# Kernel optimization log

Hardware: AMD Instinct MI355X
Metric: run time of the kernel (lower is better)

Reference implementation:

```python
import jax, jax.numpy as jnp
import numpy as np

L = 512       # sequence length
N_AA = 21     # amino-acid alphabet size
D = 128       # per-residue substitution embedding dim
N1 = 256
N2 = 256


def setup_inputs() -> dict:
    key = jax.random.key(0)
    k1, k2, k3 = jax.random.split(key, 3)
    X1 = jax.random.randint(k1, (N1, L), 0, N_AA)
    X2 = jax.random.randint(k2, (N2, L), 0, N_AA)
    W = jax.random.normal(k3, (L * N_AA, N_AA * D), dtype=jnp.float32) * 0.02
    b = jnp.zeros((N_AA * D,), jnp.float32)
    w_param = jnp.zeros((L * (L - 1) // 2,), jnp.float32)
    a = jnp.ones((1,), jnp.float32)
    return {"X1": X1, "X2": X2, "W": W, "b": b, "w_param": w_param, "a": a}


def _network(X, W, b):
    # one-hot + linear stand-in for self.network; outputs (n, n_aa, d)
    n = X.shape[0]
    oh = jax.nn.one_hot(X, N_AA, dtype=W.dtype).reshape(n, -1)  # (n, L*n_aa)
    return (oh @ W + b).reshape(n, N_AA, -1)


def _wdk(subs, w):
    # torch: (subs[:, graph] * w).sum(2) * subs, summed over dim 1
    # graph[i] = arange(L), so this equals subs @ w^T contracted with subs:
    # out[..] = sum_i sum_j subs[.., i] * w[i, j] * subs[.., j]
    return jnp.einsum('...i,ij,...j->...', subs, w, subs)


def reference(X1, X2, W, b, w_param, a):
    n1, Lx = X1.shape
    n2 = X2.shape[0]

    # symmetric pairwise weight matrix; diagonal stays 0 -> sigmoid(0)=0.5
    i_x, i_y = np.tril_indices(Lx, k=-1)
    wm = jnp.zeros((Lx, Lx), W.dtype).at[i_x, i_y].set(w_param).at[i_y, i_x].set(w_param)
    w = jax.nn.sigmoid(wm)

    # per-sequence substitution matrices S = E E^T, (n, n_aa, n_aa)
    E1 = _network(X1, W, b)
    S1 = jnp.einsum('nad,nbd->nab', E1, E1)
    E2 = _network(X2, W, b)
    S2 = jnp.einsum('nad,nbd->nab', E2, E2)

    r1 = jnp.arange(n1)
    r2 = jnp.arange(n2)

    # self terms: subs[n, l] = S[n, X[n,l], X[n,l]]
    d1 = S1[r1[:, None], X1, X1]                  # (n1, L)
    k1 = _wdk(d1, w)[:, None]                     # (n1, 1)
    d2 = S2[r2[:, None], X2, X2]                  # (n2, L)
    k2 = _wdk(d2, w)[None, :]                     # (1, n2)

    # cross terms: average of the two sequences' S, gathered directly
    # (avoids materializing the (n1*n2, n_aa, n_aa) averaged S tensor)
    g1 = S1[r1[:, None, None], X1[:, None, :], X2[None, :, :]]  # (n1, n2, L)
    g2 = S2[r2[None, :, None], X1[:, None, :], X2[None, :, :]]  # (n1, n2, L)
    subs = 0.5 * (g1 + g2)

    K = _wdk(subs, w)                             # (n1, n2)
    K = K / jnp.sqrt(k1) / jnp.sqrt(k2)
    return (a ** 2) * K
```

## Files before the change

kernel.cpp:

```cpp
#include <hip/hip_runtime.h>
#include <cstdint>
#include <cstddef>

typedef __attribute__((ext_vector_type(8))) __bf16 bf16x8;
typedef __attribute__((ext_vector_type(4))) float f32x4;
typedef __attribute__((ext_vector_type(16))) float f32x16;

__device__ __forceinline__ unsigned short f2b(float x) {
    uint32_t u = __float_as_uint(x);
    u += 0x7FFFu + ((u >> 16) & 1u);
    return (unsigned short)(u >> 16);
}
__device__ __forceinline__ float b2f(unsigned short h) {
    return __uint_as_float(((uint32_t)h) << 16);
}

#define L_SEQ 512
#define N_AA 21
#define DDIM 128
#define NCOL 2688
#define NSEQ 512
#define TBSTRIDE 448
#define KTOT 10752
#define ZCH 12
#define KBTOT 672
#define KBCH 56

#define PB_WBZ   14112
#define PB_EINIT 5376
#define PB_REPACK 1024
#define PB_WBUILD 1024
#define PB_ABZ   2688
#define PB_TOTAL (PB_WBZ + PB_EINIT + PB_REPACK + PB_WBUILD + PB_ABZ)

__global__ __launch_bounds__(256) void prep_kernel(const int* X1, const int* X2,
                                                   const float* W, const float* bvec, const float* wp,
                                                   uint8_t* X8,
                                                   float* w32, unsigned short* wswz,
                                                   float* E, unsigned short* Wbz, unsigned short* Abz) {
    int bid = blockIdx.x;
    int t = threadIdx.x;
    if (bid < PB_WBZ) {
        int f = bid * 4 + (t >> 6);
        int lane = t & 63, lr = lane & 31, hf = lane >> 5;
        int cb = f / KBTOT, kb = f - cb * KBTOT;
        const float* src = W + (size_t)(kb * 16 + hf * 8) * NCOL + cb * 32 + lr;
        union { uint4 q; unsigned short s[8]; } o;
#pragma unroll
        for (int j = 0; j < 8; ++j) o.s[j] = f2b(src[(size_t)j * NCOL]);
        *(uint4*)&Wbz[(size_t)f * 512 + lane * 8] = o.q;
        return;
    }
    bid -= PB_WBZ;
    if (bid < PB_EINIT) {
        int e = bid * 256 + t;
        E[e] = bvec[e % NCOL];
        return;
    }
    bid -= PB_EINIT;
    if (bid < PB_REPACK) {
        int e = bid * 256 + t;
        if (e < 131072) X8[e] = (uint8_t)X1[e];
        else            X8[e] = (uint8_t)X2[e - 131072];
        return;
    }
    bid -= PB_REPACK;
    if (bid < PB_WBUILD) {
        int e = bid * 256 + t;
        int p = e >> 9, q = e & 511;
        float x = 0.0f;
        if (p > q)      x = wp[p * (p - 1) / 2 + q];
        else if (p < q) x = wp[q * (q - 1) / 2 + p];
        float s = 1.0f / (1.0f + expf(-x));
        w32[e] = s;
        int nb = p >> 5, lr = p & 31;
        int kb = q >> 4, hf = (q >> 3) & 1, j = q & 7;
        wswz[(size_t)((nb * 32 + kb) * 512) + (hf * 32 + lr) * 8 + j] = f2b(s);
        return;
    }
    bid -= PB_WBUILD;
    {
        int f = bid * 4 + (t >> 6);
        int lane = t & 63, lr = lane & 31, hf = lane >> 5;
        int mb = f / KBTOT, kb = f - mb * KBTOT;
        int m = mb * 32 + lr;
        const int* Xrow = (m < 256) ? (X1 + (size_t)m * L_SEQ) : (X2 + (size_t)(m - 256) * L_SEQ);
        int k0 = kb * 16 + hf * 8;
        union { uint4 q; unsigned short s[8]; } o;
#pragma unroll
        for (int j = 0; j < 8; ++j) {
            int k = k0 + j;
            int l = k / N_AA;
            int aa = k - l * N_AA;
            o.s[j] = (Xrow[l] == aa) ? (unsigned short)0x3F80u : (unsigned short)0u;
        }
        *(uint4*)&Abz[(size_t)f * 512 + lane * 8] = o.q;
    }
}

__global__ __launch_bounds__(256, 4) void e_mfma_v2(const unsigned short* Abz, const unsigned short* Wbz, float* E) {
    int lin = blockIdx.x;
    int s = ((lin & 7) * 126) + (lin >> 3);
    int cx = s % 21;
    int rem = s / 21;
    int my = rem & 3;
    int kz = rem >> 2;

    int t = threadIdx.x, wid = t >> 6, lane = t & 63;
    int lr = lane & 31, hf = lane >> 5;

    int kb0 = kz * KBCH;
    int mb0 = my * 4 + (wid & 1) * 2;
    int cb0 = cx * 4 + (wid >> 1) * 2;

    const unsigned short* Ap0 = Abz + ((size_t)(mb0 * KBTOT + kb0)) * 512 + lane * 8;
    const unsigned short* Ap1 = Ap0 + (size_t)KBTOT * 512;
    const unsigned short* Bp0 = Wbz + ((size_t)(cb0 * KBTOT + kb0)) * 512 + lane * 8;
    const unsigned short* Bp1 = Bp0 + (size_t)KBTOT * 512;

    f32x16 acc00, acc01, acc10, acc11;
#pragma unroll
    for (int r = 0; r < 16; ++r) { acc00[r] = 0.f; acc01[r] = 0.f; acc10[r] = 0.f; acc11[r] = 0.f; }

#pragma unroll 2
    for (int kb = 0; kb < KBCH; ++kb) {
        bf16x8 a0 = *(const bf16x8*)(Ap0 + kb * 512);
        bf16x8 a1 = *(const bf16x8*)(Ap1 + kb * 512);
        bf16x8 b0 = *(const bf16x8*)(Bp0 + kb * 512);
        bf16x8 b1 = *(const bf16x8*)(Bp1 + kb * 512);
        acc00 = __builtin_amdgcn_mfma_f32_32x32x16_bf16(a0, b0, acc00, 0, 0, 0);
        acc01 = __builtin_amdgcn_mfma_f32_32x32x16_bf16(a0, b1, acc01, 0, 0, 0);
        acc10 = __builtin_amdgcn_mfma_f32_32x32x16_bf16(a1, b0, acc10, 0, 0, 0);
        acc11 = __builtin_amdgcn_mfma_f32_32x32x16_bf16(a1, b1, acc11, 0, 0, 0);
    }

#pragma unroll
    for (int r = 0; r < 16; ++r) {
        int row = (r & 3) + 8 * (r >> 2) + 4 * hf;
        float* base = E + (size_t)(mb0 * 32 + row) * NCOL + cb0 * 32 + lr;
        atomicAdd(base, acc00[r]);
        atomicAdd(base + 32, acc01[r]);
        atomicAdd(base + (size_t)32 * NCOL, acc10[r]);
        atomicAdd(base + (size_t)32 * NCOL + 32, acc11[r]);
    }
}

__global__ __launch_bounds__(256) void t_kernel(const float* E, unsigned short* Tb, float* Tdiag) {
    __shared__ float4 Es4[21 * 33];
    int t = threadIdx.x, n = blockIdx.x;
    for (int e = t; e < 21 * 32; e += 256) {
        int r = e >> 5, d = e & 31;
        Es4[r * 33 + d] = *(const float4*)(E + (size_t)n * NCOL + r * 128 + d * 4);
    }
    __syncthreads();
    for (int e = t; e < 441; e += 256) {
        int r = e / 21, c = e - r * 21;
        const float4* ar = &Es4[r * 33];
        const float4* br = &Es4[c * 33];
        float s = 0.f;
#pragma unroll 8
        for (int d = 0; d < 32; ++d) {
            float4 a = ar[d], b = br[d];
            s += a.x * b.x + a.y * b.y + a.z * b.z + a.w * b.w;
        }
        Tb[(size_t)n * TBSTRIDE + e] = f2b(0.5f * s);
        if (r == c) Tdiag[n * 24 + r] = s;
    }
}

__global__ __launch_bounds__(256) void k_kernel(const uint8_t* X8, const float* Tdiag, const float* w32, float* kinv) {
    __shared__ __align__(16) float dvec[4][512];
    __shared__ float Td[4][21];
    __shared__ float red[4][256];
    int t = threadIdx.x, n0 = blockIdx.x * 4;
    if (t < 84) Td[t / 21][t % 21] = Tdiag[(size_t)(n0 + t / 21) * 24 + (t % 21)];
    __syncthreads();
    for (int e = t; e < 2048; e += 256) {
        int nn = e >> 9, l = e & 511;
        dvec[nn][l] = Td[nn][X8[(size_t)(n0 + nn) * 512 + l]];
    }
    __syncthreads();
    float p0 = 0.f, p1 = 0.f, p2 = 0.f, p3 = 0.f;
    for (int p = t; p < 512; p += 256) {
        const float4* wr4 = (const float4*)(w32 + (size_t)p * 512);
        float d0 = 0.f, d1 = 0.f, d2 = 0.f, d3 = 0.f;
        for (int q = 0; q < 128; ++q) {
            float4 wv = wr4[q];
            float4 a = ((const float4*)dvec[0])[q];
            float4 b = ((const float4*)dvec[1])[q];
            float4 c = ((const float4*)dvec[2])[q];
            float4 d = ((const float4*)dvec[3])[q];
            d0 += wv.x * a.x + wv.y * a.y + wv.z * a.z + wv.w * a.w;
            d1 += wv.x * b.x + wv.y * b.y + wv.z * b.z + wv.w * b.w;
            d2 += wv.x * c.x + wv.y * c.y + wv.z * c.z + wv.w * c.w;
            d3 += wv.x * d.x + wv.y * d.y + wv.z * d.z + wv.w * d.w;
        }
        p0 += dvec[0][p] * d0;
        p1 += dvec[1][p] * d1;
        p2 += dvec[2][p] * d2;
        p3 += dvec[3][p] * d3;
    }
    red[0][t] = p0; red[1][t] = p1; red[2][t] = p2; red[3][t] = p3;
    __syncthreads();
    for (int s = 128; s > 0; s >>= 1) {
        if (t < s) {
            red[0][t] += red[0][t + s];
            red[1][t] += red[1][t + s];
            red[2][t] += red[2][t + s];
            red[3][t] += red[3][t + s];
        }
        __syncthreads();
    }
    if (t < 4) kinv[n0 + t] = 1.0f / sqrtf(red[t][0]);
}

__global__ __launch_bounds__(512, 6) void k4_kernel(const uint8_t* X8, const unsigned short* Tb,
                                                    const unsigned short* wswz, const float* kinv,
                                                    const float* Ainp, float* out) {
    __shared__ unsigned short Sh[32 * 520];
    __shared__ unsigned short Ts1h[4 * TBSTRIDE];
    __shared__ unsigned short Ts2h[8 * TBSTRIDE];
    __shared__ unsigned short A21[4 * 512];
    __shared__ uint8_t Xs2[8 * 512];
    __shared__ float Kacc[8][32];

    int t = threadIdx.x;
    int i0 = blockIdx.x * 4;
    int j0 = blockIdx.y * 8;

    for (int e = t; e < 4 * 512; e += 512)
        A21[e] = (unsigned short)(21 * X8[(size_t)(i0 + (e >> 9)) * 512 + (e & 511)]);
    {
        const uint32_t* s2 = (const uint32_t*)(X8 + (size_t)(256 + j0) * 512);
        uint32_t* d2 = (uint32_t*)Xs2;
        for (int e = t; e < 1024; e += 512) d2[e] = s2[e];
    }
    {
        uint32_t* d1 = (uint32_t*)Ts1h;
        for (int e = t; e < 4 * 224; e += 512) {
            int r = e / 224, w = e - r * 224;
            d1[e] = ((const uint32_t*)(Tb + (size_t)(i0 + r) * TBSTRIDE))[w];
        }
        uint32_t* d2 = (uint32_t*)Ts2h;
        for (int e = t; e < 8 * 224; e += 512) {
            int r = e / 224, w = e - r * 224;
            d2[e] = ((const uint32_t*)(Tb + (size_t)(256 + j0 + r) * TBSTRIDE))[w];
        }
    }
    __syncthreads();

    for (int e4 = t; e4 < 32 * 128; e4 += 512) {
        int pr = e4 >> 7, p = (e4 & 127) * 4;
        int ti = pr >> 3, tj = pr & 7;
        uint64_t a4 = *(const uint64_t*)&A21[ti * 512 + p];
        uint32_t b4 = *(const uint32_t*)&Xs2[tj * 512 + p];
        const unsigned short* T1 = &Ts1h[ti * TBSTRIDE];
        const unsigned short* T2 = &Ts2h[tj * TBSTRIDE];
        uint64_t outw = 0;
#pragma unroll
        for (int u = 0; u < 4; ++u) {
            int idx = (int)((a4 >> (16 * u)) & 0xFFFFu) + (int)((b4 >> (8 * u)) & 0xFFu);
            float v = b2f(T1[idx]) + b2f(T2[idx]);
            outw |= (uint64_t)f2b(v) << (16 * u);
        }
        *(uint64_t*)&Sh[pr * 520 + p] = outw;
    }
    __syncthreads();

    int wid = t >> 6, lane = t & 63;
    int lr = lane & 31, hf = lane >> 5;
    int n_base = wid * 64;

    const unsigned short* Sa = &Sh[lr * 520 + hf * 8];
    const unsigned short* Bz0 = wswz + (size_t)((wid * 2 + 0) * 32) * 512 + lane * 8;
    const unsigned short* Bz1 = wswz + (size_t)((wid * 2 + 1) * 32) * 512 + lane * 8;

    f32x16 acc0, acc1;
#pragma unroll
    for (int j = 0; j < 16; ++j) { acc0[j] = 0.f; acc1[j] = 0.f; }

#pragma unroll 2
    for (int kt = 0; kt < 32; ++kt) {
        bf16x8 av = *(const bf16x8*)(Sa + kt * 16);
        bf16x8 bv0 = *(const bf16x8*)(Bz0 + kt * 512);
        bf16x8 bv1 = *(const bf16x8*)(Bz1 + kt * 512);
        acc0 = __builtin_amdgcn_mfma_f32_32x32x16_bf16(av, bv0, acc0, 0, 0, 0);
        acc1 = __builtin_amdgcn_mfma_f32_32x32x16_bf16(av, bv1, acc1, 0, 0, 0);
    }

    float prow[16];
#pragma unroll
    for (int r = 0; r < 16; ++r) {
        int row = (r & 3) + 8 * (r >> 2) + 4 * hf;
        float v = acc0[r] * b2f(Sh[row * 520 + (n_base + lr)]);
        v      += acc1[r] * b2f(Sh[row * 520 + (n_base + 32 + lr)]);
        prow[r] = v;
    }
#pragma unroll
    for (int r = 0; r < 16; ++r) {
        float v = prow[r];
        v += __shfl_xor(v, 1);
        v += __shfl_xor(v, 2);
        v += __shfl_xor(v, 4);
        v += __shfl_xor(v, 8);
        v += __shfl_xor(v, 16);
        if (lr == 0) {
            int row = (r & 3) + 8 * (r >> 2) + 4 * hf;
            Kacc[wid][row] = v;
        }
    }
    __syncthreads();

    if (t < 32) {
        float K = Kacc[0][t] + Kacc[1][t] + Kacc[2][t] + Kacc[3][t]
                + Kacc[4][t] + Kacc[5][t] + Kacc[6][t] + Kacc[7][t];
        int ti = t >> 3, tj = t & 7;
        int i = i0 + ti, j = j0 + tj;
        float a0 = Ainp[0];
        out[i * 256 + j] = a0 * a0 * K * kinv[i] * kinv[256 + j];
    }
}

extern "C" void kernel_launch(void* const* d_in, const int* in_sizes, int n_in,
                              void* d_out, int out_size, void* d_ws, size_t ws_size,
                              hipStream_t stream) {
    const int*   X1 = (const int*)d_in[0];
    const int*   X2 = (const int*)d_in[1];
    const float* W  = (const float*)d_in[2];
    const float* b  = (const float*)d_in[3];
    const float* wp = (const float*)d_in[4];
    const float* a  = (const float*)d_in[5];
    float* out = (float*)d_out;

    char* ws = (char*)d_ws;
    float*          E     = (float*)(ws + 0);
    unsigned short* Tb    = (unsigned short*)(ws + 5505024);
    float*          Tdiag = (float*)(ws + 5963776);
    float*          w32   = (float*)(ws + 6012928);
    unsigned short* wswz  = (unsigned short*)(ws + 7061504);
    float*          kinv  = (float*)(ws + 7585792);
    uint8_t*        X8    = (uint8_t*)(ws + 7587840);
    unsigned short* Abz   = (unsigned short*)(ws + 7849984);
    unsigned short* Wbz   = (unsigned short*)(ws + 18860032);

    prep_kernel<<<PB_TOTAL, 256, 0, stream>>>(X1, X2, W, b, wp, X8, w32, wswz, E, Wbz, Abz);
    e_mfma_v2<<<1008, 256, 0, stream>>>(Abz, Wbz, E);
    t_kernel<<<512, 256, 0, stream>>>(E, Tb, Tdiag);
    k_kernel<<<128, 256, 0, stream>>>(X8, Tdiag, w32, kinv);
    k4_kernel<<<dim3(64, 32), 512, 0, stream>>>(X8, Tb, wswz, kinv, a, out);
}
```

Before: 382.7 us.

## Stage E-GEMM operands through LDS with async global_load_lds quad-buffering

The E projection GEMM kernel previously had each wave load its A and B fragments straight from global memory, so neighbouring waves fetched the same fragments twice. It now stages A and B tiles into a 4-deep LDS ring with async global-to-LDS loads, keeping three k-blocks in flight. Each wave loads one fragment and the block shares it, which halves global traffic and overlaps loads with MFMA. In exchange it adds two workgroup barriers per k-step and 32 KB of LDS per block, which may limit occupancy.

Result: no change. 376.3 us (-1.7%).

```diff
diff --git a/kernel.cpp b/kernel.cpp
--- a/kernel.cpp
+++ b/kernel.cpp
@@ -13,6 +13,11 @@
 }
 __device__ __forceinline__ float b2f(unsigned short h) {
     return __uint_as_float(((uint32_t)h) << 16);
+}
+
+__device__ __forceinline__ void gl16(const unsigned short* g, unsigned short* l) {
+    __builtin_amdgcn_global_load_lds((const __attribute__((address_space(1))) uint32_t*)g,
+                                     (__attribute__((address_space(3))) uint32_t*)l, 16, 0, 0);
 }
 
 #define L_SEQ 512
@@ -98,7 +103,9 @@
     }
 }
 
-__global__ __launch_bounds__(256, 4) void e_mfma_v2(const unsigned short* Abz, const unsigned short* Wbz, float* E) {
+__global__ __launch_bounds__(256, 4) void e_mfma_v3(const unsigned short* Abz, const unsigned short* Wbz, float* E) {
+    __shared__ unsigned short lds[4 * 8 * 512];
+
     int lin = blockIdx.x;
     int s = ((lin & 7) * 126) + (lin >> 3);
     int cx = s % 21;
@@ -108,32 +115,67 @@
 
     int t = threadIdx.x, wid = t >> 6, lane = t & 63;
     int lr = lane & 31, hf = lane >> 5;
-
     int kb0 = kz * KBCH;
+
+    const unsigned short* Aw = Abz + ((size_t)((my * 4 + wid) * KBTOT + kb0)) * 512 + lane * 8;
+    const unsigned short* Bw = Wbz + ((size_t)((cx * 4 + wid) * KBTOT + kb0)) * 512 + lane * 8;
+    unsigned short* La = &lds[wid * 512];
+    unsigned short* Lb = &lds[(4 + wid) * 512];
+
+#define STG(buf_, kb_) do { \
+        gl16(Aw + (size_t)(kb_) * 512, La + (buf_) * 4096); \
+        gl16(Bw + (size_t)(kb_) * 512, Lb + (buf_) * 4096); \
+    } while (0)
+
+    int alo = (wid & 1) * 2;
+    int blo = 4 + (wid >> 1) * 2;
+
+    f32x16 acc00, acc01, acc10, acc11;
+#pragma unroll
+    for (int r = 0; r < 16; ++r) { acc00[r] = 0.f; acc01[r] = 0.f; acc10[r] = 0.f; acc11[r] = 0.f; }
+
+#define COMPUTE(kb_) do { \
+        const unsigned short* base = &lds[((kb_) & 3) * 4096]; \
+        bf16x8 a0 = *(const bf16x8*)(base + (alo + 0) * 512 + lane * 8); \
+        bf16x8 a1 = *(const bf16x8*)(base + (alo + 1) * 512 + lane * 8); \
+        bf16x8 b0 = *(const bf16x8*)(base + (blo + 0) * 512 + lane * 8); \
+        bf16x8 b1 = *(const bf16x8*)(base + (blo + 1) * 512 + lane * 8); \
+        acc00 = __builtin_amdgcn_mfma_f32_32x32x16_bf16(a0, b0, acc00, 0, 0, 0); \
+        acc01 = __builtin_amdgcn_mfma_f32_32x32x16_bf16(a0, b1, acc01, 0, 0, 0); \
+        acc10 = __builtin_amdgcn_mfma_f32_32x32x16_bf16(a1, b0, acc10, 0, 0, 0); \
+        acc11 = __builtin_amdgcn_mfma_f32_32x32x16_bf16(a1, b1, acc11, 0, 0, 0); \
+    } while (0)
+
+    STG(0, 0); STG(1, 1); STG(2, 2);
+
+#pragma unroll 1
+    for (int kb = 0; kb < KBCH - 3; ++kb) {
+        STG((kb + 3) & 3, kb + 3);
+        asm volatile("s_waitcnt vmcnt(6)" ::: "memory");
+        __builtin_amdgcn_s_barrier();
+        __builtin_amdgcn_sched_barrier(0);
+        COMPUTE(kb);
+        __builtin_amdgcn_sched_barrier(0);
+        __builtin_amdgcn_s_barrier();
+    }
+    asm volatile("s_waitcnt vmcnt(4)" ::: "memory");
+    __builtin_amdgcn_s_barrier();
+    __builtin_amdgcn_sched_barrier(0);
+    COMPUTE(53);
+    asm volatile("s_waitcnt vmcnt(2)" ::: "memory");
+    __builtin_amdgcn_s_barrier();
+    __builtin_amdgcn_sched_barrier(0);
+    COMPUTE(54);
+    asm volatile("s_waitcnt vmcnt(0)" ::: "memory");
+    __builtin_amdgcn_s_barrier();
+    __builtin_amdgcn_sched_barrier(0);
+    COMPUTE(55);
+
+#undef STG
+#undef COMPUTE
+
     int mb0 = my * 4 + (wid & 1) * 2;
     int cb0 = cx * 4 + (wid >> 1) * 2;
-
-    const unsigned short* Ap0 = Abz + ((size_t)(mb0 * KBTOT + kb0)) * 512 + lane * 8;
-    const unsigned short* Ap1 = Ap0 + (size_t)KBTOT * 512;
-    const unsigned short* Bp0 = Wbz + ((size_t)(cb0 * KBTOT + kb0)) * 512 + lane * 8;
-    const unsigned short* Bp1 = Bp0 + (size_t)KBTOT * 512;
-
-    f32x16 acc00, acc01, acc10, acc11;
-#pragma unroll
-    for (int r = 0; r < 16; ++r) { acc00[r] = 0.f; acc01[r] = 0.f; acc10[r] = 0.f; acc11[r] = 0.f; }
-
-#pragma unroll 2
-    for (int kb = 0; kb < KBCH; ++kb) {
-        bf16x8 a0 = *(const bf16x8*)(Ap0 + kb * 512);
-        bf16x8 a1 = *(const bf16x8*)(Ap1 + kb * 512);
-        bf16x8 b0 = *(const bf16x8*)(Bp0 + kb * 512);
-        bf16x8 b1 = *(const bf16x8*)(Bp1 + kb * 512);
-        acc00 = __builtin_amdgcn_mfma_f32_32x32x16_bf16(a0, b0, acc00, 0, 0, 0);
-        acc01 = __builtin_amdgcn_mfma_f32_32x32x16_bf16(a0, b1, acc01, 0, 0, 0);
-        acc10 = __builtin_amdgcn_mfma_f32_32x32x16_bf16(a1, b0, acc10, 0, 0, 0);
-        acc11 = __builtin_amdgcn_mfma_f32_32x32x16_bf16(a1, b1, acc11, 0, 0, 0);
-    }
-
 #pragma unroll
     for (int r = 0; r < 16; ++r) {
         int row = (r & 3) + 8 * (r >> 2) + 4 * hf;
@@ -344,7 +386,7 @@
     unsigned short* Wbz   = (unsigned short*)(ws + 18860032);
 
     prep_kernel<<<PB_TOTAL, 256, 0, stream>>>(X1, X2, W, b, wp, X8, w32, wswz, E, Wbz, Abz);
-    e_mfma_v2<<<1008, 256, 0, stream>>>(Abz, Wbz, E);
+    e_mfma_v3<<<1008, 256, 0, stream>>>(Abz, Wbz, E);
     t_kernel<<<512, 256, 0, stream>>>(E, Tb, Tdiag);
     k_kernel<<<128, 256, 0, stream>>>(X8, Tdiag, w32, kinv);
     k4_kernel<<<dim3(64, 32), 512, 0, stream>>>(X8, Tb, wswz, kinv, a, out);
```
